# Kernel optimization log

Hardware: AMD Instinct MI355X
Metric: run time of the kernel (lower is better)

Reference implementation:

```python
import jax, jax.numpy as jnp
import numpy as np

N_NODES = 100000


def gcn_conv(x, edge_index, W, b):
    """PyG-style GCNConv: h = D^-1/2 (A+I) D^-1/2 (x W) + b."""
    n = x.shape[0]
    loop = jnp.arange(n)
    src = jnp.concatenate([edge_index[0], loop])  # [E+N]
    dst = jnp.concatenate([edge_index[1], loop])  # [E+N]
    # degree computed on destination nodes (PyG gcn_norm with self-loops)
    deg = jnp.zeros((n,), x.dtype).at[dst].add(1.0)
    dinv = jnp.where(deg > 0, jax.lax.rsqrt(deg), 0.0)
    norm = dinv[src] * dinv[dst]  # [E+N]
    h = x @ W  # [n, out]
    msg = h[src] * norm[:, None]  # gather + scale
    out = jax.ops.segment_sum(msg, dst, num_segments=n)  # scatter-add
    return out + b


def setup_inputs() -> dict:
    key = jax.random.key(0)
    ks = jax.random.split(key, 8)
    F_in, H, C = 64, 64, 32
    x = jax.random.normal(ks[0], (N_NODES, F_in), dtype=jnp.float32)
    edge_index = jax.random.randint(ks[1], (2, 1200000), 0, N_NODES, dtype=jnp.int64)
    W1 = jax.random.normal(ks[2], (F_in, H), dtype=jnp.float32) / np.sqrt(F_in)
    b1 = jnp.zeros((H,), jnp.float32)
    W2 = jax.random.normal(ks[3], (H, H), dtype=jnp.float32) / np.sqrt(H)
    b2 = jnp.zeros((H,), jnp.float32)
    Wc = jax.random.normal(ks[4], (H, C), dtype=jnp.float32) / np.sqrt(H)
    bc = jnp.zeros((C,), jnp.float32)
    return {"x": x, "edge_index": edge_index, "W1": W1, "b1": b1,
            "W2": W2, "b2": b2, "Wc": Wc, "bc": bc}


def reference(x, edge_index, W1, b1, W2, b2, Wc, bc):
    h = jnp.tanh(gcn_conv(x, edge_index, W1, b1))
    h = jnp.tanh(gcn_conv(h, edge_index, W2, b2))
    out = h @ Wc + bc
    return (out, h)
```

## Files before the change

### kernel.cpp

```cpp
#include <hip/hip_runtime.h>
#include <hip/hip_bf16.h>
#include <stdint.h>

#define CB_SHIFT 11
#define CB_NODES 2048
#define CAP 28672
#define PT 4096

static __device__ inline uint16_t f2bf(float f) {
    union { float f; uint32_t u; } v; v.f = f;
    uint32_t r = v.u + 0x7FFFu + ((v.u >> 16) & 1u);
    return (uint16_t)(r >> 16);
}
static __device__ inline float bflo(uint32_t u) {
    union { uint32_t u; float f; } v; v.u = u << 16; return v.f;
}
static __device__ inline float bfhi(uint32_t u) {
    union { uint32_t u; float f; } v; v.u = u & 0xFFFF0000u; return v.f;
}
static __device__ inline float tanh_fast(float x) {
    x = fminf(fmaxf(x, -20.f), 20.f);
    float e = __expf(2.f * x);
    return fmaf(-2.f, __builtin_amdgcn_rcpf(e + 1.f), 1.f);
}

__global__ __launch_bounds__(256) void k_init(const uint32_t* __restrict__ e, int E,
                                              int* __restrict__ flag, int* __restrict__ gcur,
                                              int* __restrict__ dhist) {
    int t = threadIdx.x;
    dhist[t] = 0;
    if (t < 64) {
        gcur[t] = 0;
        int cnt = E < 1024 ? E : 1024;
        int nz = 0;
        for (int i = t; i < cnt; i += 64) nz |= (e[2 * i + 1] != 0u);
        int any = __any(nz);
        if (t == 0) *flag = any ? 0 : 1;
    }
}

__global__ __launch_bounds__(256) void k_part(const uint32_t* __restrict__ e, int E,
                                              const int* __restrict__ flag,
                                              int* __restrict__ gcur,
                                              uint32_t* __restrict__ parts) {
    __shared__ int sh_hist[64], sh_off[64], sh_base[64];
    __shared__ uint32_t sh_buf[PT];
    __shared__ uint16_t sh_bkt[PT];
    int t = threadIdx.x;
    int tile0 = blockIdx.x * PT;
    int is64 = *flag;
    if (t < 64) sh_hist[t] = 0;
    __syncthreads();

    uint32_t rec[16]; int cb[16], rank[16];
    const uint2* e2p = (const uint2*)e;
    for (int j = 0; j < 16; ++j) {
        int idx = tile0 + j * 256 + t;
        cb[j] = -1;
        if (idx < E) {
            uint32_t s, d;
            if (is64) { s = e2p[idx].x; d = e2p[E + idx].x; }
            else      { s = e[idx];     d = e[E + idx]; }
            rec[j] = (s << CB_SHIFT) | (d & (CB_NODES - 1));
            cb[j] = (int)(d >> CB_SHIFT);
            rank[j] = atomicAdd(&sh_hist[cb[j]], 1);
        }
    }
    __syncthreads();
    if (t < 64) {
        int cnt = sh_hist[t];
        int incl = cnt;
        for (int o = 1; o < 64; o <<= 1) {
            int v = __shfl_up(incl, o);
            if (t >= o) incl += v;
        }
        sh_off[t] = incl - cnt;
        sh_base[t] = (cnt > 0) ? atomicAdd(&gcur[t], cnt) : 0;
    }
    __syncthreads();
    for (int j = 0; j < 16; ++j) {
        if (cb[j] >= 0) {
            int slot = sh_off[cb[j]] + rank[j];
            sh_buf[slot] = rec[j];
            sh_bkt[slot] = (uint16_t)cb[j];
        }
    }
    __syncthreads();
    int total = min(PT, E - tile0);
    for (int i = t; i < total; i += 256) {
        int b = sh_bkt[i];
        int dest = sh_base[b] + (i - sh_off[b]);
        parts[(size_t)b * CAP + dest] = sh_buf[i];
    }
}

__global__ __launch_bounds__(1024) void k_build(const uint32_t* __restrict__ parts,
                                                const int* __restrict__ gcur,
                                                float* __restrict__ dinv,
                                                int* __restrict__ rowbeg,
                                                int* __restrict__ rowend,
                                                uint32_t* __restrict__ col,
                                                int* __restrict__ dhist, int N) {
    __shared__ int hist[CB_NODES], cur[CB_NODES], wsum[16], dh[256];
    int t = threadIdx.x, cb = blockIdx.x;
    int lane = t & 63, w = t >> 6;
    for (int i = t; i < CB_NODES; i += 1024) hist[i] = 0;
    if (t < 256) dh[t] = 0;
    __syncthreads();
    int cnt = gcur[cb];
    const uint32_t* rp = parts + (size_t)cb * CAP;
    for (int i = t; i < cnt; i += 1024) atomicAdd(&hist[rp[i] & (CB_NODES - 1)], 1);
    __syncthreads();
    int h0 = hist[2 * t], h1 = hist[2 * t + 1];
    int n0 = cb * CB_NODES;
    if (n0 + 2 * t < N)     atomicAdd(&dh[min(h0, 255)], 1);
    if (n0 + 2 * t + 1 < N) atomicAdd(&dh[min(h1, 255)], 1);
    int s = h0 + h1;
    int incl = s;
    for (int o = 1; o < 64; o <<= 1) {
        int v = __shfl_up(incl, o);
        if (lane >= o) incl += v;
    }
    if (lane == 63) wsum[w] = incl;
    __syncthreads();
    if (t < 16) {
        int v = wsum[t];
        int inc2 = v;
        for (int o = 1; o < 16; o <<= 1) {
            int u = __shfl_up(inc2, o);
            if (t >= o) inc2 += u;
        }
        wsum[t] = inc2 - v;
    }
    __syncthreads();
    int ex = wsum[w] + incl - s;
    int b0 = ex, b1 = ex + h0;
    cur[2 * t] = b0;
    cur[2 * t + 1] = b1;
    int base = cb * CAP;
    if (n0 + 2 * t < N) {
        rowbeg[n0 + 2 * t] = base + b0;
        rowend[n0 + 2 * t] = base + b0 + h0;
        dinv[n0 + 2 * t] = rsqrtf((float)(h0 + 1));
    }
    if (n0 + 2 * t + 1 < N) {
        rowbeg[n0 + 2 * t + 1] = base + b1;
        rowend[n0 + 2 * t + 1] = base + b1 + h1;
        dinv[n0 + 2 * t + 1] = rsqrtf((float)(h1 + 1));
    }
    __syncthreads();
    if (t < 256 && dh[t]) atomicAdd(&dhist[t], dh[t]);
    for (int i = t; i < cnt; i += 1024) {
        uint32_t rec = rp[i];
        int pos = atomicAdd(&cur[rec & (CB_NODES - 1)], 1);
        col[base + pos] = rec >> CB_SHIFT;
    }
}

__global__ __launch_bounds__(256) void k_dscan(const int* __restrict__ dhist,
                                               int* __restrict__ dcur) {
    __shared__ int sd[256];
    int t = threadIdx.x;
    int v = dhist[t];
    sd[t] = v; __syncthreads();
    for (int o = 1; o < 256; o <<= 1) {
        int x = (t >= o) ? sd[t - o] : 0;
        __syncthreads();
        sd[t] += x;
        __syncthreads();
    }
    dcur[t] = sd[t] - v;
}

__global__ __launch_bounds__(1024) void k_dperm(const int* __restrict__ rowbeg,
                                                const int* __restrict__ rowend,
                                                const float* __restrict__ dinv,
                                                int* __restrict__ dcur,
                                                int4* __restrict__ perm4, int N) {
    __shared__ int lh[256], lbase[256];
    int t = threadIdx.x;
    if (t < 256) lh[t] = 0;
    __syncthreads();
    int n = blockIdx.x * 1024 + t;
    int c = 0, rank = 0, beg = 0, deg = 0;
    if (n < N) {
        beg = rowbeg[n];
        deg = rowend[n] - beg;
        c = min(deg, 255);
        rank = atomicAdd(&lh[c], 1);
    }
    __syncthreads();
    if (t < 256 && lh[t]) lbase[t] = atomicAdd(&dcur[t], lh[t]);
    __syncthreads();
    if (n < N) {
        int pos = lbase[c] + rank;
        perm4[(N - 1) - pos] = make_int4(beg, deg, n, __float_as_int(dinv[n]));
    }
}

__global__ __launch_bounds__(256) void k_gemm(const float* __restrict__ A,
                                              const float* __restrict__ W,
                                              const float* __restrict__ dinv,
                                              uint16_t* __restrict__ out, int N) {
    __shared__ __align__(16) float xT[64 * 68];
    __shared__ __align__(16) float Wl[64 * 64];
    int t = threadIdx.x;
#pragma unroll
    for (int j = 0; j < 16; ++j) Wl[j * 256 + t] = W[j * 256 + t];
    int n0 = blockIdx.x * 64;
    int nvalid = min(64, N - n0);
#pragma unroll
    for (int j = 0; j < 4; ++j) {
        int flat = j * 256 + t;
        int node = flat >> 4;
        int k4 = (flat & 15) * 4;
        float4 v = make_float4(0.f, 0.f, 0.f, 0.f);
        if (node < nvalid) v = *(const float4*)&A[(size_t)(n0 + node) * 64 + k4];
        xT[(k4 + 0) * 68 + node] = v.x;
        xT[(k4 + 1) * 68 + node] = v.y;
        xT[(k4 + 2) * 68 + node] = v.z;
        xT[(k4 + 3) * 68 + node] = v.w;
    }
    __syncthreads();
    int ng = t >> 4, cg = t & 15;
    float acc[4][4] = {};
#pragma unroll 8
    for (int k = 0; k < 64; ++k) {
        float4 a = *(const float4*)&xT[k * 68 + 4 * ng];
        float4 b = *(const float4*)&Wl[k * 64 + 4 * cg];
        float av[4] = {a.x, a.y, a.z, a.w};
        float bv[4] = {b.x, b.y, b.z, b.w};
#pragma unroll
        for (int i = 0; i < 4; ++i)
#pragma unroll
            for (int j = 0; j < 4; ++j) acc[i][j] = fmaf(av[i], bv[j], acc[i][j]);
    }
#pragma unroll
    for (int i = 0; i < 4; ++i) {
        int ln = 4 * ng + i;
        if (ln < nvalid) {
            int n = n0 + ln;
            float dv = dinv[n];
            ushort4 o;
            o.x = f2bf(acc[i][0] * dv);
            o.y = f2bf(acc[i][1] * dv);
            o.z = f2bf(acc[i][2] * dv);
            o.w = f2bf(acc[i][3] * dv);
            *(ushort4*)&out[(size_t)n * 64 + 4 * cg] = o;
        }
    }
}

__global__ __launch_bounds__(512) void k_agg(const uint16_t* __restrict__ h,
                                             const int4* __restrict__ perm4,
                                             const uint32_t* __restrict__ col,
                                             const float* __restrict__ bias,
                                             float* __restrict__ out, int N) {
    int t = threadIdx.x;
    int lane = t & 63, wid = t >> 6;
    int slot = lane >> 4;
    int sub  = (lane >> 3) & 1;
    int g = lane & 7;
    const uint4* hp = (const uint4*)h;
    float bv[4];
#pragma unroll
    for (int j = 0; j < 4; ++j) bv[j] = bias[g * 8 + sub * 4 + j];
    int idx = (blockIdx.x * 8 + wid) * 4 + slot;
    bool valid = idx < N;
    int4 pi = make_int4(0, 0, 0, 0);
    if (valid) pi = perm4[idx];
    int rs = pi.x, deg = valid ? pi.y : 0, n = pi.z;
    float di = __int_as_float(pi.w);
    int m = deg;
#pragma unroll
    for (int o = 1; o < 64; o <<= 1) m = max(m, __shfl_xor(m, o));
    int trips = (m + 1) >> 1;
    float acc[8] = {};
#pragma unroll 4
    for (int it = 0; it < trips; ++it) {
        int e = 2 * it + sub;
        if (e < deg) {
            int src = (int)col[rs + e];
            uint4 v = hp[(size_t)src * 8 + g];
            acc[0] += bflo(v.x); acc[1] += bfhi(v.x);
            acc[2] += bflo(v.y); acc[3] += bfhi(v.y);
            acc[4] += bflo(v.z); acc[5] += bfhi(v.z);
            acc[6] += bflo(v.w); acc[7] += bfhi(v.w);
        }
    }
#pragma unroll
    for (int j = 0; j < 8; ++j) acc[j] += __shfl_xor(acc[j], 8);
    if (valid) {
        float s0 = sub ? acc[4] : acc[0];
        float s1 = sub ? acc[5] : acc[1];
        float s2 = sub ? acc[6] : acc[2];
        float s3 = sub ? acc[7] : acc[3];
        uint2 v = *(const uint2*)&h[(size_t)n * 64 + g * 8 + sub * 4];
        float hn0 = bflo(v.x), hn1 = bfhi(v.x), hn2 = bflo(v.y), hn3 = bfhi(v.y);
        __align__(16) float o[4];
        o[0] = tanh_fast(di * (s0 + hn0) + bv[0]);
        o[1] = tanh_fast(di * (s1 + hn1) + bv[1]);
        o[2] = tanh_fast(di * (s2 + hn2) + bv[2]);
        o[3] = tanh_fast(di * (s3 + hn3) + bv[3]);
        *(float4*)&out[(size_t)n * 64 + g * 8 + sub * 4] = *(float4*)&o[0];
    }
}

__global__ __launch_bounds__(256) void k_cls(const float* __restrict__ A,
                                             const float* __restrict__ W,
                                             const float* __restrict__ bc,
                                             float* __restrict__ out, int N) {
    __shared__ __align__(16) float xT[64 * 68];
    __shared__ __align__(16) float Wl[64 * 32];
    int t = threadIdx.x;
#pragma unroll
    for (int j = 0; j < 8; ++j) Wl[j * 256 + t] = W[j * 256 + t];
    int n0 = blockIdx.x * 64;
    int nvalid = min(64, N - n0);
#pragma unroll
    for (int j = 0; j < 4; ++j) {
        int flat = j * 256 + t;
        int node = flat >> 4;
        int k4 = (flat & 15) * 4;
        float4 v = make_float4(0.f, 0.f, 0.f, 0.f);
        if (node < nvalid) v = *(const float4*)&A[(size_t)(n0 + node) * 64 + k4];
        xT[(k4 + 0) * 68 + node] = v.x;
        xT[(k4 + 1) * 68 + node] = v.y;
        xT[(k4 + 2) * 68 + node] = v.z;
        xT[(k4 + 3) * 68 + node] = v.w;
    }
    __syncthreads();
    int ng = t >> 4, cg = t & 15;
    float acc[4][2] = {};
#pragma unroll 8
    for (int k = 0; k < 64; ++k) {
        float4 a = *(const float4*)&xT[k * 68 + 4 * ng];
        float2 b = *(const float2*)&Wl[k * 32 + 2 * cg];
        float av[4] = {a.x, a.y, a.z, a.w};
#pragma unroll
        for (int i = 0; i < 4; ++i) {
            acc[i][0] = fmaf(av[i], b.x, acc[i][0]);
            acc[i][1] = fmaf(av[i], b.y, acc[i][1]);
        }
    }
    float2 bcv = *(const float2*)&bc[2 * cg];
#pragma unroll
    for (int i = 0; i < 4; ++i) {
        int ln = 4 * ng + i;
        if (ln < nvalid) {
            int n = n0 + ln;
            float2 o = make_float2(acc[i][0] + bcv.x, acc[i][1] + bcv.y);
            *(float2*)&out[(size_t)n * 32 + 2 * cg] = o;
        }
    }
}

extern "C" void kernel_launch(void* const* d_in, const int* in_sizes, int n_in,
                              void* d_out, int out_size, void* d_ws, size_t ws_size,
                              hipStream_t stream) {
    const float*    x     = (const float*)d_in[0];
    const uint32_t* edges = (const uint32_t*)d_in[1];
    const float*    W1    = (const float*)d_in[2];
    const float*    b1    = (const float*)d_in[3];
    const float*    W2    = (const float*)d_in[4];
    const float*    b2    = (const float*)d_in[5];
    const float*    Wc    = (const float*)d_in[6];
    const float*    bc    = (const float*)d_in[7];

    const int N   = in_sizes[0] / 64;
    const int E   = in_sizes[1] / 2;
    const int NBC = (N + CB_NODES - 1) >> CB_SHIFT;
    const int NTG = (N + 63) / 64;
    const int NTP = (E + PT - 1) / PT;
    const int NAG = (N + 31) / 32;
    const int NDP = (N + 1023) / 1024;

    char* w = (char*)d_ws;
    size_t off = 0;
    auto alloc = [&](size_t bytes) {
        void* p = w + off;
        off = (off + bytes + 255) & ~(size_t)255;
        return p;
    };
    int*      flag   = (int*)alloc(4);
    int*      gcur   = (int*)alloc(64 * 4);
    int*      dhist  = (int*)alloc(256 * 4);
    int*      dcur   = (int*)alloc(256 * 4);
    float*    dinv   = (float*)alloc((size_t)N * 4);
    uint32_t* parts  = (uint32_t*)alloc((size_t)NBC * CAP * 4);
    uint32_t* col    = (uint32_t*)alloc((size_t)NBC * CAP * 4);
    int*      rowbeg = (int*)alloc((size_t)N * 4);
    int*      rowend = (int*)alloc((size_t)N * 4);
    int4*     perm4  = (int4*)alloc((size_t)N * 16);
    uint16_t* bufA   = (uint16_t*)alloc((size_t)N * 64 * 2);

    float* outc = (float*)d_out;
    float* hfin = outc + (size_t)N * 32;

    hipLaunchKernelGGL(k_init, dim3(1), dim3(256), 0, stream, edges, E, flag, gcur, dhist);
    hipLaunchKernelGGL(k_part, dim3(NTP), dim3(256), 0, stream, edges, E, flag, gcur, parts);
    hipLaunchKernelGGL(k_build, dim3(NBC), dim3(1024), 0, stream, parts, gcur, dinv, rowbeg, rowend, col, dhist, N);
    hipLaunchKernelGGL(k_dscan, dim3(1), dim3(256), 0, stream, dhist, dcur);
    hipLaunchKernelGGL(k_dperm, dim3(NDP), dim3(1024), 0, stream, rowbeg, rowend, dinv, dcur, perm4, N);

    hipLaunchKernelGGL(k_gemm, dim3(NTG), dim3(256), 0, stream, x, W1, dinv, bufA, N);
    hipLaunchKernelGGL(k_agg, dim3(NAG), dim3(512), 0, stream, bufA, perm4, col, b1, hfin, N);
    hipLaunchKernelGGL(k_gemm, dim3(NTG), dim3(256), 0, stream, hfin, W2, dinv, bufA, N);
    hipLaunchKernelGGL(k_agg, dim3(NAG), dim3(512), 0, stream, bufA, perm4, col, b2, hfin, N);
    hipLaunchKernelGGL(k_cls, dim3(NTG), dim3(256), 0, stream, hfin, Wc, bc, outc, N);
}
```

Baseline: 255.5 us.

## Use finer dst buckets with LDS staging and bf16 intermediate hidden layer

Shrinks destination buckets from 2048 to 256 nodes, giving 512 partitions and a two-level scan in the partition kernel. The CSR build now stages the column array in LDS and writes it out contiguously instead of scattering it to global memory. The first layer's output is stored as bf16 in a scratch buffer and the second GEMM reads bf16, halving that round trip. It also reuses the parts buffer for perm4 and raises the aggregation unroll factor. The cost is lower precision in the intermediate activations and more global atomics on the bucket counters.

```diff
diff --git a/kernel.cpp b/kernel.cpp
--- a/kernel.cpp
+++ b/kernel.cpp
@@ -2,9 +2,10 @@
 #include <hip/hip_bf16.h>
 #include <stdint.h>
 
-#define CB_SHIFT 11
-#define CB_NODES 2048
-#define CAP 28672
+#define CB_SHIFT 8
+#define CB_NODES 256
+#define CAP 3584
+#define NBINS 512
 #define PT 4096
 
 static __device__ inline uint16_t f2bf(float f) {
@@ -18,6 +19,9 @@
 static __device__ inline float bfhi(uint32_t u) {
     union { uint32_t u; float f; } v; v.u = u & 0xFFFF0000u; return v.f;
 }
+static __device__ inline float bfu(uint16_t u) {
+    union { uint32_t u; float f; } v; v.u = ((uint32_t)u) << 16; return v.f;
+}
 static __device__ inline float tanh_fast(float x) {
     x = fminf(fmaxf(x, -20.f), 20.f);
     float e = __expf(2.f * x);
@@ -29,8 +33,9 @@
                                               int* __restrict__ dhist) {
     int t = threadIdx.x;
     dhist[t] = 0;
+    gcur[t] = 0;
+    gcur[256 + t] = 0;
     if (t < 64) {
-        gcur[t] = 0;
         int cnt = E < 1024 ? E : 1024;
         int nz = 0;
         for (int i = t; i < cnt; i += 64) nz |= (e[2 * i + 1] != 0u);
@@ -43,13 +48,14 @@
                                               const int* __restrict__ flag,
                                               int* __restrict__ gcur,
                                               uint32_t* __restrict__ parts) {
-    __shared__ int sh_hist[64], sh_off[64], sh_base[64];
+    __shared__ int sh_hist[NBINS], sh_off[NBINS], sh_base[NBINS], pw[4];
     __shared__ uint32_t sh_buf[PT];
     __shared__ uint16_t sh_bkt[PT];
     int t = threadIdx.x;
     int tile0 = blockIdx.x * PT;
     int is64 = *flag;
-    if (t < 64) sh_hist[t] = 0;
+    sh_hist[t] = 0;
+    sh_hist[256 + t] = 0;
     __syncthreads();
 
     uint32_t rec[16]; int cb[16], rank[16];
@@ -67,15 +73,29 @@
         }
     }
     __syncthreads();
-    if (t < 64) {
-        int cnt = sh_hist[t];
-        int incl = cnt;
+    int c0 = sh_hist[2 * t], c1 = sh_hist[2 * t + 1];
+    int s2 = c0 + c1;
+    int incl = s2;
+    {
+        int lane = t & 63;
         for (int o = 1; o < 64; o <<= 1) {
             int v = __shfl_up(incl, o);
-            if (t >= o) incl += v;
-        }
-        sh_off[t] = incl - cnt;
-        sh_base[t] = (cnt > 0) ? atomicAdd(&gcur[t], cnt) : 0;
+            if (lane >= o) incl += v;
+        }
+        if (lane == 63) pw[t >> 6] = incl;
+    }
+    __syncthreads();
+    if (t == 0) {
+        int r = 0;
+        for (int k = 0; k < 4; ++k) { int v = pw[k]; pw[k] = r; r += v; }
+    }
+    __syncthreads();
+    {
+        int ex = pw[t >> 6] + incl - s2;
+        sh_off[2 * t] = ex;
+        sh_off[2 * t + 1] = ex + c0;
+        sh_base[2 * t]     = c0 ? atomicAdd(&gcur[2 * t], c0) : 0;
+        sh_base[2 * t + 1] = c1 ? atomicAdd(&gcur[2 * t + 1], c1) : 0;
     }
     __syncthreads();
     for (int j = 0; j < 16; ++j) {
@@ -94,67 +114,61 @@
     }
 }
 
-__global__ __launch_bounds__(1024) void k_build(const uint32_t* __restrict__ parts,
-                                                const int* __restrict__ gcur,
-                                                float* __restrict__ dinv,
-                                                int* __restrict__ rowbeg,
-                                                int* __restrict__ rowend,
-                                                uint32_t* __restrict__ col,
-                                                int* __restrict__ dhist, int N) {
-    __shared__ int hist[CB_NODES], cur[CB_NODES], wsum[16], dh[256];
+__global__ __launch_bounds__(512) void k_build(const uint32_t* __restrict__ parts,
+                                               const int* __restrict__ gcur,
+                                               float* __restrict__ dinv,
+                                               int* __restrict__ rowbeg,
+                                               int* __restrict__ rowend,
+                                               uint32_t* __restrict__ col,
+                                               int* __restrict__ dhist, int N) {
+    __shared__ int hist[CB_NODES], cur[CB_NODES], dh[256], wsum4[4];
+    __shared__ uint32_t sbuf[CAP];
     int t = threadIdx.x, cb = blockIdx.x;
-    int lane = t & 63, w = t >> 6;
-    for (int i = t; i < CB_NODES; i += 1024) hist[i] = 0;
-    if (t < 256) dh[t] = 0;
+    if (t < 256) { hist[t] = 0; dh[t] = 0; }
     __syncthreads();
     int cnt = gcur[cb];
     const uint32_t* rp = parts + (size_t)cb * CAP;
-    for (int i = t; i < cnt; i += 1024) atomicAdd(&hist[rp[i] & (CB_NODES - 1)], 1);
-    __syncthreads();
-    int h0 = hist[2 * t], h1 = hist[2 * t + 1];
-    int n0 = cb * CB_NODES;
-    if (n0 + 2 * t < N)     atomicAdd(&dh[min(h0, 255)], 1);
-    if (n0 + 2 * t + 1 < N) atomicAdd(&dh[min(h1, 255)], 1);
-    int s = h0 + h1;
-    int incl = s;
-    for (int o = 1; o < 64; o <<= 1) {
-        int v = __shfl_up(incl, o);
-        if (lane >= o) incl += v;
-    }
-    if (lane == 63) wsum[w] = incl;
-    __syncthreads();
-    if (t < 16) {
-        int v = wsum[t];
-        int inc2 = v;
-        for (int o = 1; o < 16; o <<= 1) {
-            int u = __shfl_up(inc2, o);
-            if (t >= o) inc2 += u;
-        }
-        wsum[t] = inc2 - v;
-    }
-    __syncthreads();
-    int ex = wsum[w] + incl - s;
-    int b0 = ex, b1 = ex + h0;
-    cur[2 * t] = b0;
-    cur[2 * t + 1] = b1;
-    int base = cb * CAP;
-    if (n0 + 2 * t < N) {
-        rowbeg[n0 + 2 * t] = base + b0;
-        rowend[n0 + 2 * t] = base + b0 + h0;
-        dinv[n0 + 2 * t] = rsqrtf((float)(h0 + 1));
-    }
-    if (n0 + 2 * t + 1 < N) {
-        rowbeg[n0 + 2 * t + 1] = base + b1;
-        rowend[n0 + 2 * t + 1] = base + b1 + h1;
-        dinv[n0 + 2 * t + 1] = rsqrtf((float)(h1 + 1));
+    for (int i = t; i < cnt; i += 512) atomicAdd(&hist[rp[i] & (CB_NODES - 1)], 1);
+    __syncthreads();
+    int h = 0, incl = 0;
+    if (t < 256) {
+        h = hist[t];
+        int lane = t & 63;
+        incl = h;
+        for (int o = 1; o < 64; o <<= 1) {
+            int v = __shfl_up(incl, o);
+            if (lane >= o) incl += v;
+        }
+        if (lane == 63) wsum4[t >> 6] = incl;
+    }
+    __syncthreads();
+    if (t == 0) {
+        int r = 0;
+        for (int k = 0; k < 4; ++k) { int v = wsum4[k]; wsum4[k] = r; r += v; }
+    }
+    __syncthreads();
+    if (t < 256) {
+        int ex = wsum4[t >> 6] + incl - h;
+        cur[t] = ex;
+        int n = cb * CB_NODES + t;
+        int base = cb * CAP;
+        if (n < N) {
+            rowbeg[n] = base + ex;
+            rowend[n] = base + ex + h;
+            dinv[n] = rsqrtf((float)(h + 1));
+            atomicAdd(&dh[min(h, 255)], 1);
+        }
     }
     __syncthreads();
     if (t < 256 && dh[t]) atomicAdd(&dhist[t], dh[t]);
-    for (int i = t; i < cnt; i += 1024) {
+    for (int i = t; i < cnt; i += 512) {
         uint32_t rec = rp[i];
         int pos = atomicAdd(&cur[rec & (CB_NODES - 1)], 1);
-        col[base + pos] = rec >> CB_SHIFT;
-    }
+        sbuf[pos] = rec >> CB_SHIFT;
+    }
+    __syncthreads();
+    int base = cb * CAP;
+    for (int i = t; i < cnt; i += 512) col[base + i] = sbuf[i];
 }
 
 __global__ __launch_bounds__(256) void k_dscan(const int* __restrict__ dhist,
@@ -198,7 +212,8 @@
     }
 }
 
-__global__ __launch_bounds__(256) void k_gemm(const float* __restrict__ A,
+template<int ABF16>
+__global__ __launch_bounds__(256) void k_gemm(const void* __restrict__ Ap,
                                               const float* __restrict__ W,
                                               const float* __restrict__ dinv,
                                               uint16_t* __restrict__ out, int N) {
@@ -215,7 +230,14 @@
         int node = flat >> 4;
         int k4 = (flat & 15) * 4;
         float4 v = make_float4(0.f, 0.f, 0.f, 0.f);
-        if (node < nvalid) v = *(const float4*)&A[(size_t)(n0 + node) * 64 + k4];
+        if (node < nvalid) {
+            if (ABF16) {
+                ushort4 u = *((const ushort4*)Ap + ((size_t)(n0 + node) * 16 + (k4 >> 2)));
+                v = make_float4(bfu(u.x), bfu(u.y), bfu(u.z), bfu(u.w));
+            } else {
+                v = *(const float4*)((const float*)Ap + (size_t)(n0 + node) * 64 + k4);
+            }
+        }
         xT[(k4 + 0) * 68 + node] = v.x;
         xT[(k4 + 1) * 68 + node] = v.y;
         xT[(k4 + 2) * 68 + node] = v.z;
@@ -251,20 +273,21 @@
     }
 }
 
+template<int OBF16>
 __global__ __launch_bounds__(512) void k_agg(const uint16_t* __restrict__ h,
                                              const int4* __restrict__ perm4,
                                              const uint32_t* __restrict__ col,
                                              const float* __restrict__ bias,
-                                             float* __restrict__ out, int N) {
+                                             void* __restrict__ out, int N) {
     int t = threadIdx.x;
     int lane = t & 63, wid = t >> 6;
-    int slot = lane >> 4;
     int sub  = (lane >> 3) & 1;
     int g = lane & 7;
     const uint4* hp = (const uint4*)h;
     float bv[4];
 #pragma unroll
     for (int j = 0; j < 4; ++j) bv[j] = bias[g * 8 + sub * 4 + j];
+    int slot = lane >> 4;
     int idx = (blockIdx.x * 8 + wid) * 4 + slot;
     bool valid = idx < N;
     int4 pi = make_int4(0, 0, 0, 0);
@@ -276,7 +299,7 @@
     for (int o = 1; o < 64; o <<= 1) m = max(m, __shfl_xor(m, o));
     int trips = (m + 1) >> 1;
     float acc[8] = {};
-#pragma unroll 4
+#pragma unroll 8
     for (int it = 0; it < trips; ++it) {
         int e = 2 * it + sub;
         if (e < deg) {
@@ -297,12 +320,18 @@
         float s3 = sub ? acc[7] : acc[3];
         uint2 v = *(const uint2*)&h[(size_t)n * 64 + g * 8 + sub * 4];
         float hn0 = bflo(v.x), hn1 = bfhi(v.x), hn2 = bflo(v.y), hn3 = bfhi(v.y);
-        __align__(16) float o[4];
-        o[0] = tanh_fast(di * (s0 + hn0) + bv[0]);
-        o[1] = tanh_fast(di * (s1 + hn1) + bv[1]);
-        o[2] = tanh_fast(di * (s2 + hn2) + bv[2]);
-        o[3] = tanh_fast(di * (s3 + hn3) + bv[3]);
-        *(float4*)&out[(size_t)n * 64 + g * 8 + sub * 4] = *(float4*)&o[0];
+        float r0 = tanh_fast(di * (s0 + hn0) + bv[0]);
+        float r1 = tanh_fast(di * (s1 + hn1) + bv[1]);
+        float r2 = tanh_fast(di * (s2 + hn2) + bv[2]);
+        float r3 = tanh_fast(di * (s3 + hn3) + bv[3]);
+        if (OBF16) {
+            ushort4 ob;
+            ob.x = f2bf(r0); ob.y = f2bf(r1); ob.z = f2bf(r2); ob.w = f2bf(r3);
+            *(ushort4*)&((uint16_t*)out)[(size_t)n * 64 + g * 8 + sub * 4] = ob;
+        } else {
+            __align__(16) float o[4] = {r0, r1, r2, r3};
+            *(float4*)&((float*)out)[(size_t)n * 64 + g * 8 + sub * 4] = *(float4*)&o[0];
+        }
     }
 }
 
@@ -383,7 +412,7 @@
         return p;
     };
     int*      flag   = (int*)alloc(4);
-    int*      gcur   = (int*)alloc(64 * 4);
+    int*      gcur   = (int*)alloc(NBINS * 4);
     int*      dhist  = (int*)alloc(256 * 4);
     int*      dcur   = (int*)alloc(256 * 4);
     float*    dinv   = (float*)alloc((size_t)N * 4);
@@ -391,21 +420,26 @@
     uint32_t* col    = (uint32_t*)alloc((size_t)NBC * CAP * 4);
     int*      rowbeg = (int*)alloc((size_t)N * 4);
     int*      rowend = (int*)alloc((size_t)N * 4);
-    int4*     perm4  = (int4*)alloc((size_t)N * 16);
     uint16_t* bufA   = (uint16_t*)alloc((size_t)N * 64 * 2);
+    uint16_t* bufB   = (uint16_t*)alloc((size_t)N * 64 * 2);
+    int4*     perm4  = (int4*)parts;
 
     float* outc = (float*)d_out;
     float* hfin = outc + (size_t)N * 32;
 
     hipLaunchKernelGGL(k_init, dim3(1), dim3(256), 0, stream, edges, E, flag, gcur, dhist);
     hipLaunchKernelGGL(k_part, dim3(NTP), dim3(256), 0, stream, edges, E, flag, gcur, parts);
-    hipLaunchKernelGGL(k_build, dim3(NBC), dim3(1024), 0, stream, parts, gcur, dinv, rowbeg, rowend, col, dhist, N);
+    hipLaunchKernelGGL(k_build, dim3(NBC), dim3(512), 0, stream, parts, gcur, dinv, rowbeg, rowend, col, dhist, N);
     hipLaunchKernelGGL(k_dscan, dim3(1), dim3(256), 0, stream, dhist, dcur);
     hipLaunchKernelGGL(k_dperm, dim3(NDP), dim3(1024), 0, stream, rowbeg, rowend, dinv, dcur, perm4, N);
 
-    hipLaunchKernelGGL(k_gemm, dim3(NTG), dim3(256), 0, stream, x, W1, dinv, bufA, N);
-    hipLaunchKernelGGL(k_agg, dim3(NAG), dim3(512), 0, stream, bufA, perm4, col, b1, hfin, N);
-    hipLaunchKernelGGL(k_gemm, dim3(NTG), dim3(256), 0, stream, hfin, W2, dinv, bufA, N);
-    hipLaunchKernelGGL(k_agg, dim3(NAG), dim3(512), 0, stream, bufA, perm4, col, b2, hfin, N);
+    hipLaunchKernelGGL(HIP_KERNEL_NAME(k_gemm<0>), dim3(NTG), dim3(256), 0, stream,
+                       (const void*)x, W1, dinv, bufA, N);
+    hipLaunchKernelGGL(HIP_KERNEL_NAME(k_agg<1>), dim3(NAG), dim3(512), 0, stream,
+                       bufA, perm4, col, b1, (void*)bufB, N);
+    hipLaunchKernelGGL(HIP_KERNEL_NAME(k_gemm<1>), dim3(NTG), dim3(256), 0, stream,
+                       (const void*)bufB, W2, dinv, bufA, N);
+    hipLaunchKernelGGL(HIP_KERNEL_NAME(k_agg<0>), dim3(NAG), dim3(512), 0, stream,
+                       bufA, perm4, col, b2, (void*)hfin, N);
     hipLaunchKernelGGL(k_cls, dim3(NTG), dim3(256), 0, stream, hfin, Wc, bc, outc, N);
 }
```

New measurement: 243.7 us. -4.6%, faster.
